# Kernel tuning notes

Measured on AMD Instinct MI355X. Metric: run time of the kernel, lower is better.

The kernel has to match this reference:

```python
import jax, jax.numpy as jnp
import numpy as np

HID = 768      # hidden_dim
HEADS = 12     # num_heads (each head projects HID -> HID, unsplit)
NP_ = 196      # num_patches = (224/16)^2
PATCH = 256    # 1*16*16
SEQ = NP_ + 1  # +CLS
OUT = 1000
BLOCKS = 6
EPS = 1e-5


def setup_inputs() -> dict:
    key = jax.random.key(0)
    ks = jax.random.split(key, 12)
    def w(k, shape, s=0.02):
        return jax.random.normal(k, shape, jnp.float32) * s
    return {
        "X": jax.random.normal(ks[0], (8, 1, 224, 224), jnp.float32),
        "W_patch": w(ks[1], (HID, PATCH)), "b_patch": jnp.zeros((HID,), jnp.float32),
        "cls_emb": jax.random.uniform(ks[2], (1, HID), jnp.float32),
        "pos_emb": jax.random.uniform(ks[3], (SEQ, HID), jnp.float32),
        "ln1_g": jnp.ones((SEQ, HID), jnp.float32), "ln1_b": jnp.zeros((SEQ, HID), jnp.float32),
        "Wq": w(ks[4], (HEADS, HID, HID)), "bq": jnp.zeros((HEADS, HID), jnp.float32),
        "Wk": w(ks[5], (HEADS, HID, HID)), "bk": jnp.zeros((HEADS, HID), jnp.float32),
        "Wv": w(ks[6], (HEADS, HID, HID)), "bv": jnp.zeros((HEADS, HID), jnp.float32),
        "Wo": w(ks[7], (HID, HEADS * HID)), "bo": jnp.zeros((HID,), jnp.float32),
        "ln2_g": jnp.ones((SEQ, HID), jnp.float32), "ln2_b": jnp.zeros((SEQ, HID), jnp.float32),
        "W2": w(ks[8], (HID, HID)), "b2": jnp.zeros((HID,), jnp.float32),
        "Wh": w(ks[9], (OUT, HID)), "bh": jnp.zeros((OUT,), jnp.float32),
    }


def _ln2d(x, g, b):
    # torch nn.LayerNorm((SEQ, HID)): normalize over the last TWO dims
    m = x.mean(axis=(-2, -1), keepdims=True)
    v = x.var(axis=(-2, -1), keepdims=True)
    return (x - m) / jnp.sqrt(v + EPS) * g + b


def reference(X, W_patch, b_patch, cls_emb, pos_emb, ln1_g, ln1_b,
              Wq, bq, Wk, bk, Wv, bv, Wo, bo, ln2_g, ln2_b, W2, b2, Wh, bh):
    N = X.shape[0]
    patches = X.reshape(N, NP_, PATCH)
    E = patches @ W_patch.T + b_patch                      # [N, 196, HID]
    cls = jnp.broadcast_to(cls_emb[None], (N, 1, HID))
    Z = jnp.concatenate([cls, E], axis=1) + pos_emb[None]  # [N, SEQ, HID]
    scale = 1.0 / (HID ** 2)                               # repo's unusual scaling
    for _ in range(BLOCKS):  # same weights reused each iteration (as in source)
        x = _ln2d(Z, ln1_g, ln1_b)
        # batched per-head full-width projections: Wq[h] is (out=e, in=d)
        q = jnp.einsum('nsd,hed->nhse', x, Wq) + bq[None, :, None, :]
        k = jnp.einsum('nsd,hed->nhse', x, Wk) + bk[None, :, None, :]
        v = jnp.einsum('nsd,hed->nhse', x, Wv) + bv[None, :, None, :]
        A = jax.nn.softmax(jnp.einsum('nhse,nhte->nhst', q, k) * scale, axis=-1)
        h = jnp.einsum('nhst,nhte->nhse', A, v)            # [N, HEADS, SEQ, HID]
        hcat = jnp.transpose(h, (0, 2, 1, 3)).reshape(N, SEQ, HEADS * HID)
        attn = hcat @ Wo.T + bo                            # [N, SEQ, HID]
        y = _ln2d(attn + Z, ln2_g, ln2_b)
        Z = y @ W2.T + b2                                  # note: no residual here (as in source)
    return jnp.tanh(Z[:, 0] @ Wh.T + bh)                   # [N, OUT]
```

## Files before the change

### kernel.cpp

```cpp
#include <hip/hip_runtime.h>
#include <hip/hip_bf16.h>
#include <math.h>

typedef __hip_bfloat16 bf16;
typedef __attribute__((ext_vector_type(8))) short short8;
typedef __attribute__((ext_vector_type(4))) float f32x4;

#define HIDD   768
#define SEQL   197
#define NPATCH 196
#define PATCHD 256
#define NHEADS 12
#define NBATCH 8
#define OUTDIM 1000
#define NBLOCKS 6
#define EPSV   1e-5f
#define HH     (NHEADS * HIDD)
#define M_ALL  (NBATCH * SEQL)
#define MPATCH (NBATCH * NPATCH)
#define PLD    256
#define KPV    224
#define KSPLIT 4

__device__ __forceinline__ unsigned short f2bf(float f) {
  union { bf16 h; unsigned short u; } cv; cv.h = __float2bfloat16(f); return cv.u;
}
__device__ __forceinline__ float bf2f(unsigned short u) {
  union { unsigned int i; float f; } w; w.i = ((unsigned int)u) << 16; return w.f;
}

typedef __attribute__((address_space(3))) unsigned int lds_uint;
typedef __attribute__((address_space(1))) const unsigned int g_uint;
__device__ __forceinline__ void gload16(const void* g, void* l) {
  __builtin_amdgcn_global_load_lds((g_uint*)g, (lds_uint*)l, 16, 0, 0);
}

__global__ __launch_bounds__(256) void cvt_bf(const float4* __restrict__ src,
                                              ushort4* __restrict__ dst, int n4) {
  for (int i = blockIdx.x * 256 + threadIdx.x; i < n4; i += gridDim.x * 256) {
    float4 v = src[i];
    ushort4 o;
    o.x = f2bf(v.x); o.y = f2bf(v.y); o.z = f2bf(v.z); o.w = f2bf(v.w);
    dst[i] = o;
  }
}

__global__ __launch_bounds__(256) void twk(const float* __restrict__ Wk,
                                           unsigned short* __restrict__ Wkt) {
  const long long idx = (long long)blockIdx.x * 256 + threadIdx.x;
  const int h = (int)(idx / (HIDD * HIDD));
  const int rem = (int)(idx - (long long)h * HIDD * HIDD);
  const int d = rem / HIDD, e = rem - d * HIDD;
  Wkt[idx] = f2bf(Wk[(long long)h * HIDD * HIDD + (long long)e * HIDD + d]);
}

__global__ __launch_bounds__(256) void cvec(const float* __restrict__ Wk,
    const float* __restrict__ bq, float* __restrict__ c) {
  const int h = blockIdx.z;
  const int dp = blockIdx.x * 256 + threadIdx.x;
  const float* W = Wk + (long long)h * HIDD * HIDD;
  const float* b = bq + h * HIDD;
  float s = 0.f;
  for (int e = 0; e < HIDD; ++e) s += W[(long long)e * HIDD + dp] * b[e];
  c[h * HIDD + dp] = s;
}

__global__ __launch_bounds__(256) void beff_k(const float* __restrict__ Wo,
    const float* __restrict__ bv, const float* __restrict__ bo,
    float* __restrict__ beff) {
  const int dout = blockIdx.x * 4 + (threadIdx.x >> 6);
  const int lane = threadIdx.x & 63;
  const float* row = Wo + (long long)dout * HH;
  float s = 0.f;
  for (int i = lane * 4; i < HH; i += 256) {
    float4 w = *(const float4*)(row + i);
    float4 b = *(const float4*)(bv + i);
    s += w.x * b.x + w.y * b.y + w.z * b.z + w.w * b.w;
  }
  for (int o = 32; o; o >>= 1) s += __shfl_xor(s, o, 64);
  if (lane == 0) beff[dout] = bo[dout] + s;
}

__global__ __launch_bounds__(256) void dcol(const unsigned short* __restrict__ Xn,
    const float* __restrict__ c, float* __restrict__ D) {
  const int z = blockIdx.x;
  const int n = z / NHEADS, h = z - n * NHEADS;
  const int wid = threadIdx.x >> 6, lane = threadIdx.x & 63;
  const float* ch = c + h * HIDD;
  float cc[3][4];
#pragma unroll
  for (int k = 0; k < 3; ++k)
    *(float4*)cc[k] = *(const float4*)(ch + k * 256 + lane * 4);
  const int t0 = blockIdx.y * 64 + wid * 16;
#pragma unroll
  for (int tt = 0; tt < 16; ++tt) {
    const int t = t0 + tt;
    float s = 0.f;
    if (t < SEQL) {
      const unsigned short* xr = Xn + (long long)(n * SEQL + t) * HIDD;
#pragma unroll
      for (int k = 0; k < 3; ++k) {
        ushort4 xv = *(const ushort4*)(xr + k * 256 + lane * 4);
        s += bf2f(xv.x) * cc[k][0] + bf2f(xv.y) * cc[k][1]
           + bf2f(xv.z) * cc[k][2] + bf2f(xv.w) * cc[k][3];
      }
    }
    for (int o = 32; o; o >>= 1) s += __shfl_xor(s, o, 64);
    if (lane == 0) D[z * 256 + t] = s;
  }
}

__global__ __launch_bounds__(256) void xpose(const unsigned short* __restrict__ Xn,
    unsigned short* __restrict__ Xt) {
  __shared__ unsigned short tile[64][72];
  const int n = blockIdx.z;
  const int e0 = blockIdx.x * 64, t0 = blockIdx.y * 64;
  const int tr = threadIdx.x >> 2;
  const int tc = (threadIdx.x & 3) * 16;
  const int t = t0 + tr;
#pragma unroll
  for (int j = 0; j < 2; ++j) {
    int4 v = {0, 0, 0, 0};
    if (t < SEQL)
      v = *(const int4*)(Xn + (long long)(n * SEQL + t) * HIDD + e0 + tc + j * 8);
    *(int4*)&tile[tr][tc + j * 8] = v;
  }
  __syncthreads();
  const int er = threadIdx.x >> 2;
  const int tcc = (threadIdx.x & 3) * 16;
  unsigned short tmp[16];
#pragma unroll
  for (int j = 0; j < 16; ++j) tmp[j] = tile[tcc + j][er];
  unsigned short* drow = Xt + ((long long)n * HIDD + e0 + er) * 256 + t0 + tcc;
  *(int4*)drow = *(int4*)&tmp[0];
  *(int4*)(drow + 8) = *(int4*)&tmp[8];
}

template<bool BF16C>
__global__ __launch_bounds__(512, 2) void gemm_8ph(
    const unsigned short* __restrict__ A, int lda,
    const unsigned short* __restrict__ B, int ldb,
    void* __restrict__ Cp, int ldc,
    const float* __restrict__ bias, float alpha,
    int M, int N, int K, int gy)
{
  __shared__ alignas(16) unsigned short Abuf[2 * 2 * 128 * 64];
  __shared__ alignas(16) unsigned short Bbuf[2 * 2 * 128 * 64];

  const int nwg = gridDim.x;
  const int qq = nwg >> 3, rr = nwg & 7;
  const int xcd = blockIdx.x & 7, wix = blockIdx.x >> 3;
  const int f = xcd * qq + (xcd < rr ? xcd : rr) + wix;
  const int m0 = (f % gy) * 256, n0 = (f / gy) * 256;

  const int tid = threadIdx.x;
  const int lane = tid & 63, wid = tid >> 6;
  const int wr = wid >> 2, wc = wid & 3;
  const int lr = lane & 15, g = lane >> 4;

  const int srow = tid >> 3;
  const int schunk = ((tid & 7) ^ ((tid >> 3) & 7)) * 8;
  const int wbyte = wid * 1024;
  const int axor = lr & 7;

  const int ktiles = K >> 6;

  f32x4 acc[8][4];
#pragma unroll
  for (int m = 0; m < 8; ++m)
#pragma unroll
    for (int n = 0; n < 4; ++n) acc[m][n] = (f32x4){0.f, 0.f, 0.f, 0.f};

  auto stA = [&](int kt, int h) {
    const unsigned short* src = A + (long long)(m0 + h * 128 + srow) * lda + kt * 64 + schunk;
    char* dst = (char*)Abuf + ((kt & 1) * 2 + h) * 16384 + wbyte;
    gload16(src, dst);
    gload16(src + 64ll * lda, dst + 8192);
  };
  auto stB = [&](int kt, int h) {
    const unsigned short* src = B + (long long)(n0 + h * 128 + srow) * ldb + kt * 64 + schunk;
    char* dst = (char*)Bbuf + ((kt & 1) * 2 + h) * 16384 + wbyte;
    gload16(src, dst);
    gload16(src + 64ll * ldb, dst + 8192);
  };

  stB(0, 0); stB(0, 1); stA(0, 0); stA(0, 1);
  __builtin_amdgcn_s_waitcnt(0x0F72);
  __builtin_amdgcn_sched_barrier(0);
  __builtin_amdgcn_s_barrier();
  __builtin_amdgcn_sched_barrier(0);

  for (int t = 0; t < ktiles; ++t) {
    const int d = t & 1;
    const char* Ab_ = (const char*)Abuf + (d * 2 + wr) * 16384;
    const char* Bb_ = (const char*)Bbuf + (d * 2 + (wc >> 1)) * 16384;
    const int brow = (wc & 1) * 64;
    const bool more = (t + 1 < ktiles);

    short8 a[4][2], bA[2][2], bB[2][2];

#pragma unroll
    for (int m = 0; m < 4; ++m)
#pragma unroll
      for (int ks = 0; ks < 2; ++ks)
        a[m][ks] = *(const short8*)(Ab_ + (m * 16 + lr) * 128 + ((((ks << 2) | g) ^ axor) << 4));
#pragma unroll
    for (int n = 0; n < 2; ++n)
#pragma unroll
      for (int ks = 0; ks < 2; ++ks)
        bA[n][ks] = *(const short8*)(Bb_ + (brow + n * 16 + lr) * 128 + ((((ks << 2) | g) ^ axor) << 4));
    if (more) stB(t + 1, 0);
    __builtin_amdgcn_sched_barrier(0);
    __builtin_amdgcn_s_barrier();
    __builtin_amdgcn_sched_barrier(0);
    __builtin_amdgcn_s_waitcnt(0xC07F);
    __builtin_amdgcn_sched_barrier(0);
    __builtin_amdgcn_s_setprio(1);
#pragma unroll
    for (int m = 0; m < 4; ++m)
#pragma unroll
      for (int n = 0; n < 2; ++n)
#pragma unroll
        for (int ks = 0; ks < 2; ++ks)
          acc[m][n] = __builtin_amdgcn_mfma_f32_16x16x32_bf16(a[m][ks], bA[n][ks], acc[m][n], 0, 0, 0);
    __builtin_amdgcn_s_setprio(0);
    __builtin_amdgcn_sched_barrier(0);
    __builtin_amdgcn_s_barrier();
    __builtin_amdgcn_sched_barrier(0);

#pragma unroll
    for (int n = 0; n < 2; ++n)
#pragma unroll
      for (int ks = 0; ks < 2; ++ks)
        bB[n][ks] = *(const short8*)(Bb_ + (brow + (n + 2) * 16 + lr) * 128 + ((((ks << 2) | g) ^ axor) << 4));
    if (more) stB(t + 1, 1);
    if (more) __builtin_amdgcn_s_waitcnt(0x0F74);
    else      __builtin_amdgcn_s_waitcnt(0x0F70);
    __builtin_amdgcn_sched_barrier(0);
    __builtin_amdgcn_s_barrier();
    __builtin_amdgcn_sched_barrier(0);
    __builtin_amdgcn_s_waitcnt(0xC07F);
    __builtin_amdgcn_sched_barrier(0);
    __builtin_amdgcn_s_setprio(1);
#pragma unroll
    for (int m = 0; m < 4; ++m)
#pragma unroll
      for (int n = 0; n < 2; ++n)
#pragma unroll
        for (int ks = 0; ks < 2; ++ks)
          acc[m][n + 2] = __builtin_amdgcn_mfma_f32_16x16x32_bf16(a[m][ks], bB[n][ks], acc[m][n + 2], 0, 0, 0);
    __builtin_amdgcn_s_setprio(0);
    __builtin_amdgcn_sched_barrier(0);
    __builtin_amdgcn_s_barrier();
    __builtin_amdgcn_sched_barrier(0);

#pragma unroll
    for (int m = 0; m < 4; ++m)
#pragma unroll
      for (int ks = 0; ks < 2; ++ks)
        a[m][ks] = *(const short8*)(Ab_ + (64 + m * 16 + lr) * 128 + ((((ks << 2) | g) ^ axor) << 4));
    if (more) stA(t + 1, 0);
    __builtin_amdgcn_sched_barrier(0);
    __builtin_amdgcn_s_barrier();
    __builtin_amdgcn_sched_barrier(0);
    __builtin_amdgcn_s_waitcnt(0xC07F);
    __builtin_amdgcn_sched_barrier(0);
    __builtin_amdgcn_s_setprio(1);
#pragma unroll
    for (int m = 0; m < 4; ++m)
#pragma unroll
      for (int n = 0; n < 2; ++n)
#pragma unroll
        for (int ks = 0; ks < 2; ++ks)
          acc[m + 4][n + 2] = __builtin_amdgcn_mfma_f32_16x16x32_bf16(a[m][ks], bB[n][ks], acc[m + 4][n + 2], 0, 0, 0);
    __builtin_amdgcn_s_setprio(0);
    __builtin_amdgcn_sched_barrier(0);
    __builtin_amdgcn_s_barrier();
    __builtin_amdgcn_sched_barrier(0);

    if (more) {
      stA(t + 1, 1);
      __builtin_amdgcn_s_waitcnt(0x0F72);
    }
    __builtin_amdgcn_sched_barrier(0);
    __builtin_amdgcn_s_barrier();
    __builtin_amdgcn_sched_barrier(0);
    __builtin_amdgcn_s_setprio(1);
#pragma unroll
    for (int m = 0; m < 4; ++m)
#pragma unroll
      for (int n = 0; n < 2; ++n)
#pragma unroll
        for (int ks = 0; ks < 2; ++ks)
          acc[m + 4][n] = __builtin_amdgcn_mfma_f32_16x16x32_bf16(a[m][ks], bA[n][ks], acc[m + 4][n], 0, 0, 0);
    __builtin_amdgcn_s_setprio(0);
    __builtin_amdgcn_sched_barrier(0);
    __builtin_amdgcn_s_barrier();
    __builtin_amdgcn_sched_barrier(0);
  }

#pragma unroll
  for (int m = 0; m < 8; ++m) {
#pragma unroll
    for (int n = 0; n < 4; ++n) {
      const int gn = n0 + wc * 64 + n * 16 + lr;
      const float bv = bias ? bias[gn] : 0.f;
#pragma unroll
      for (int r = 0; r < 4; ++r) {
        const int gm = m0 + wr * 128 + m * 16 + g * 4 + r;
        if (gm >= M) continue;
        const float v = acc[m][n][r] * alpha + bv;
        if constexpr (BF16C)
          ((unsigned short*)Cp)[(long long)gm * ldc + gn] = f2bf(v);
        else
          ((float*)Cp)[(long long)gm * ldc + gn] = v;
      }
    }
  }
}

template<int BM, int BN, int WGM, int WGN, bool BF16C>
__global__ __launch_bounds__(256, 2) void gemm_bt(
    const unsigned short* __restrict__ A, long long sAz1, long long sAz2, int lda,
    const unsigned short* __restrict__ B, long long sBz1, long long sBz2, int ldb,
    void* __restrict__ Cp, long long sCz1, long long sCz2, int ldc,
    const float* __restrict__ bias, int zdiv, float alpha,
    int M, int N, int K, int gy)
{
  constexpr int BK = 32;
  constexpr int VM = BM / 64 + BN / 64;
  static_assert(WGM * WGN == 4, "4 waves");
  __shared__ unsigned short As[3][BM * BK];
  __shared__ unsigned short Bs[3][BN * BK];

  const int z  = blockIdx.z;
  const int z1 = z / zdiv, z2 = z - z1 * zdiv;
  const unsigned short* Ab = A + z1 * sAz1 + z2 * sAz2;
  const unsigned short* Bb = B + z1 * sBz1 + z2 * sBz2;
  const long long coff = z1 * sCz1 + z2 * sCz2;

  const int nwg = gridDim.x;
  const int qq = nwg >> 3, rr = nwg & 7;
  const int xcd = blockIdx.x & 7, wix = blockIdx.x >> 3;
  const int f = xcd * qq + (xcd < rr ? xcd : rr) + wix;
  const int m0 = (f % gy) * BM, n0 = (f / gy) * BN;

  const int tid = threadIdx.x;
  const int lane = tid & 63, wid = tid >> 6;
  const int wr = wid / WGN, wc = wid % WGN;
  constexpr int WM = BM / WGM, WN = BN / WGN, TM = WM / 16, TN = WN / 16;
  const int lr = lane & 15, g = lane >> 4;

  const int sr = wid * 16 + (lane >> 2);
  const int sc = (((lane & 3) ^ ((lane >> 3) & 3)) * 8);
  const int wbyte = wid * 1024;

  f32x4 acc[TM][TN];
#pragma unroll
  for (int m = 0; m < TM; ++m)
#pragma unroll
    for (int n = 0; n < TN; ++n) acc[m][n] = (f32x4){0.f, 0.f, 0.f, 0.f};

  auto stage = [&](int bufi, int kt) {
    const int k0 = kt * BK;
#pragma unroll
    for (int u = 0; u < BM / 64; ++u)
      gload16(Ab + (long long)(m0 + u * 64 + sr) * lda + k0 + sc,
              (char*)&As[bufi][0] + u * 4096 + wbyte);
#pragma unroll
    for (int u = 0; u < BN / 64; ++u)
      gload16(Bb + (long long)(n0 + u * 64 + sr) * ldb + k0 + sc,
              (char*)&Bs[bufi][0] + u * 4096 + wbyte);
  };

  const int rchunk = (g ^ ((lr >> 1) & 3)) * 8;

  const int ktiles = K / BK;
  stage(0, 0);
  if (ktiles > 1) stage(1, 1);
  int cur = 0;
  for (int t = 0; t < ktiles; ++t) {
    if (t + 1 < ktiles) __builtin_amdgcn_s_waitcnt(0x0F70 | VM);
    else                __builtin_amdgcn_s_waitcnt(0x0F70);
    __builtin_amdgcn_s_barrier();
    if (t + 2 < ktiles) {
      int nb = cur + 2; if (nb >= 3) nb -= 3;
      stage(nb, t + 2);
    }
    __builtin_amdgcn_sched_barrier(0);

    short8 a[TM], b[TN];
#pragma unroll
    for (int m = 0; m < TM; ++m)
      a[m] = *(const short8*)&As[cur][(wr * WM + m * 16 + lr) * BK + rchunk];
#pragma unroll
    for (int n = 0; n < TN; ++n)
      b[n] = *(const short8*)&Bs[cur][(wc * WN + n * 16 + lr) * BK + rchunk];
#pragma unroll
    for (int m = 0; m < TM; ++m)
#pragma unroll
      for (int n = 0; n < TN; ++n)
        acc[m][n] = __builtin_amdgcn_mfma_f32_16x16x32_bf16(a[m], b[n], acc[m][n], 0, 0, 0);
    cur = (cur == 2) ? 0 : cur + 1;
  }

#pragma unroll
  for (int m = 0; m < TM; ++m) {
#pragma unroll
    for (int n = 0; n < TN; ++n) {
      const int gn = n0 + wc * WN + n * 16 + lr;
      if (gn >= N) continue;
      const float bv = bias ? bias[gn] : 0.f;
#pragma unroll
      for (int r = 0; r < 4; ++r) {
        const int gm = m0 + wr * WM + m * 16 + g * 4 + r;
        if (gm >= M) continue;
        const float v = acc[m][n][r] * alpha + bv;
        if constexpr (BF16C)
          ((unsigned short*)Cp)[coff + (long long)gm * ldc + gn] = f2bf(v);
        else
          ((float*)Cp)[coff + (long long)gm * ldc + gn] = v;
      }
    }
  }
}

__global__ __launch_bounds__(256, 2) void scores_sm(
    const unsigned short* __restrict__ U, const unsigned short* __restrict__ Xn,
    const float* __restrict__ Dv, unsigned short* __restrict__ P, float scale)
{
  constexpr int BK = 32;
  __shared__ unsigned short As[3][64 * BK];
  __shared__ unsigned short Bs[3][256 * BK];

  const int z  = blockIdx.z;
  const int z1 = z / NHEADS, z2 = z - z1 * NHEADS;
  const unsigned short* Ab = U + (long long)z1 * SEQL * HH + (long long)z2 * HIDD;
  const unsigned short* Bb = Xn + (long long)z1 * SEQL * HIDD;
  unsigned short* Pz = P + (long long)z * SEQL * PLD;

  const int m0 = blockIdx.x * 64;
  const int tid = threadIdx.x;
  const int lane = tid & 63, wid = tid >> 6;
  const int lr = lane & 15, g = lane >> 4;

  const int sr = wid * 16 + (lane >> 2);
  const int sc = (((lane & 3) ^ ((lane >> 3) & 3)) * 8);
  const int wbyte = wid * 1024;
  const int rchunk = (g ^ ((lr >> 1) & 3)) * 8;

  f32x4 acc[16];
#pragma unroll
  for (int n = 0; n < 16; ++n) acc[n] = (f32x4){0.f, 0.f, 0.f, 0.f};

  auto stage = [&](int bufi, int kt) {
    const int k0 = kt * BK;
    gload16(Ab + (long long)(m0 + sr) * HH + k0 + sc, (char*)&As[bufi][0] + wbyte);
#pragma unroll
    for (int u = 0; u < 4; ++u)
      gload16(Bb + (long long)(u * 64 + sr) * HIDD + k0 + sc,
              (char*)&Bs[bufi][0] + u * 4096 + wbyte);
  };

  const int ktiles = HIDD / BK;
  stage(0, 0);
  stage(1, 1);
  int cur = 0;
  for (int t = 0; t < ktiles; ++t) {
    if (t + 1 < ktiles) __builtin_amdgcn_s_waitcnt(0x0F75);
    else                __builtin_amdgcn_s_waitcnt(0x0F70);
    __builtin_amdgcn_s_barrier();
    if (t + 2 < ktiles) {
      int nb = cur + 2; if (nb >= 3) nb -= 3;
      stage(nb, t + 2);
    }
    __builtin_amdgcn_sched_barrier(0);

    short8 a = *(const short8*)&As[cur][(wid * 16 + lr) * BK + rchunk];
#pragma unroll
    for (int n = 0; n < 16; ++n) {
      short8 b = *(const short8*)&Bs[cur][(n * 16 + lr) * BK + rchunk];
      acc[n] = __builtin_amdgcn_mfma_f32_16x16x32_bf16(a, b, acc[n], 0, 0, 0);
    }
    cur = (cur == 2) ? 0 : cur + 1;
  }

  const float* Dz = Dv + z * 256;
  float dv[16];
#pragma unroll
  for (int n = 0; n < 16; ++n) dv[n] = Dz[n * 16 + lr];

  const int growb = m0 + wid * 16 + g * 4;
#pragma unroll
  for (int r = 0; r < 4; ++r) {
    float mx = -1e30f;
#pragma unroll
    for (int n = 0; n < 16; ++n)
      if (n * 16 + lr < SEQL) mx = fmaxf(mx, (acc[n][r] + dv[n]) * scale);
    for (int o = 1; o < 16; o <<= 1) mx = fmaxf(mx, __shfl_xor(mx, o, 64));
    float sum = 0.f;
#pragma unroll
    for (int n = 0; n < 16; ++n) {
      const float e = (n * 16 + lr < SEQL) ? __expf((acc[n][r] + dv[n]) * scale - mx) : 0.f;
      acc[n][r] = e;
      sum += e;
    }
    for (int o = 1; o < 16; o <<= 1) sum += __shfl_xor(sum, o, 64);
    const float inv = 1.f / sum;
    const int grow = growb + r;
    if (grow < SEQL) {
#pragma unroll
      for (int n = 0; n < 16; ++n)
        Pz[(long long)grow * PLD + n * 16 + lr] = f2bf(acc[n][r] * inv);
    }
  }
}

template<int BM, int BN, bool BF16C>
__global__ __launch_bounds__(256) void gemm_nn(
    const unsigned short* __restrict__ A, long long sAz1, long long sAz2, int lda,
    const unsigned short* __restrict__ Bb, long long sBz1, long long sBz2, int ldb,
    void* __restrict__ Cp, long long sCz1, long long sCz2, int ldc,
    const float* __restrict__ bias, int zdiv, float alpha,
    int M, int N, int K, int Kvalid)
{
  constexpr int BK = 32;
  constexpr int LP = 40;
  __shared__ unsigned short As[BM * LP];
  __shared__ unsigned short Bs[BN * LP];

  const int z  = blockIdx.z;
  const int z1 = z / zdiv, z2 = z - z1 * zdiv;
  const unsigned short* Ab = A + z1 * sAz1 + z2 * sAz2;
  const unsigned short* Bp = Bb + z1 * sBz1 + z2 * sBz2;
  const long long coff = z1 * sCz1 + z2 * sCz2;

  const int tid = threadIdx.x;
  const int m0 = blockIdx.y * BM, n0 = blockIdx.x * BN;
  const int lane = tid & 63, wid = tid >> 6;
  const int wr = wid >> 1, wc = wid & 1;
  constexpr int WM = BM / 2, WN = BN / 2, TM = WM / 16, TN = WN / 16;
  const int lr = lane & 15, g = lane >> 4;
  const int srow = tid >> 2, scg = tid & 3;

  f32x4 acc[TM][TN];
#pragma unroll
  for (int m = 0; m < TM; ++m)
#pragma unroll
    for (int n = 0; n < TN; ++n) acc[m][n] = (f32x4){0.f, 0.f, 0.f, 0.f};

  for (int k0 = 0; k0 < K; k0 += BK) {
#pragma unroll
    for (int u = 0; u < BM / 64; ++u) {
      const int row = u * 64 + srow;
      const int gm = m0 + row;
      int4 val = {0, 0, 0, 0};
      if (gm < M)
        val = *(const int4*)(Ab + (long long)gm * lda + k0 + scg * 8);
      *(int4*)&As[row * LP + scg * 8] = val;
    }
    {
      constexpr int CH = BN / 8;
      constexpr int KP = BK / 2;
      static_assert(KP * CH <= 256, "staging exceeds block");
      if (tid < KP * CH) {
        const int kp = tid / CH;
        const int c8 = (tid - kp * CH) * 8;
        const int gn = n0 + c8;
        const int gk0 = k0 + 2 * kp;
        unsigned short r0[8] = {0,0,0,0,0,0,0,0};
        unsigned short r1[8] = {0,0,0,0,0,0,0,0};
        if (gk0 < Kvalid) {
          if (gn + 7 < N) *(int4*)r0 = *(const int4*)(Bp + (long long)gk0 * ldb + gn);
          else { for (int j = 0; j < 8; ++j) if (gn + j < N) r0[j] = Bp[(long long)gk0 * ldb + gn + j]; }
        }
        if (gk0 + 1 < Kvalid) {
          if (gn + 7 < N) *(int4*)r1 = *(const int4*)(Bp + (long long)(gk0 + 1) * ldb + gn);
          else { for (int j = 0; j < 8; ++j) if (gn + j < N) r1[j] = Bp[(long long)(gk0 + 1) * ldb + gn + j]; }
        }
#pragma unroll
        for (int j = 0; j < 8; ++j)
          *(unsigned int*)&Bs[(c8 + j) * LP + 2 * kp] =
              (unsigned int)r0[j] | ((unsigned int)r1[j] << 16);
      }
    }
    __syncthreads();

    short8 a[TM], b[TN];
#pragma unroll
    for (int m = 0; m < TM; ++m)
      a[m] = *(const short8*)&As[(wr * WM + m * 16 + lr) * LP + g * 8];
#pragma unroll
    for (int n = 0; n < TN; ++n)
      b[n] = *(const short8*)&Bs[(wc * WN + n * 16 + lr) * LP + g * 8];
#pragma unroll
    for (int m = 0; m < TM; ++m)
#pragma unroll
      for (int n = 0; n < TN; ++n)
        acc[m][n] = __builtin_amdgcn_mfma_f32_16x16x32_bf16(a[m], b[n], acc[m][n], 0, 0, 0);
    __syncthreads();
  }

#pragma unroll
  for (int m = 0; m < TM; ++m) {
#pragma unroll
    for (int n = 0; n < TN; ++n) {
      const int gn = n0 + wc * WN + n * 16 + lr;
      if (gn >= N) continue;
      const float bv = bias ? bias[gn] : 0.f;
#pragma unroll
      for (int r = 0; r < 4; ++r) {
        const int gm = m0 + wr * WM + m * 16 + g * 4 + r;
        if (gm >= M) continue;
        const float v = acc[m][n][r] * alpha + bv;
        if constexpr (BF16C)
          ((unsigned short*)Cp)[coff + (long long)gm * ldc + gn] = f2bf(v);
        else
          ((float*)Cp)[coff + (long long)gm * ldc + gn] = v;
      }
    }
  }
}

template<int BM, int BN>
__global__ __launch_bounds__(256) void gemm_k(
    const float* __restrict__ A, long long sAz1, int lda,
    const float* __restrict__ B, int ldb,
    float* __restrict__ C, long long sCz1, int ldc,
    const float* __restrict__ bias,
    const float* __restrict__ resid, int ldr,
    float alpha, int M, int N, int K, int act)
{
  constexpr int BK = 16;
  constexpr int TM = BM / 16;
  constexpr int TN = BN / 16;
  __shared__ float As[BK][BM];
  __shared__ float Bs[BK][BN];

  const int z = blockIdx.z;
  A += z * sAz1;
  C += z * sCz1;
  const float* R = resid;

  const int tid = threadIdx.x;
  const int tx = tid & 15, ty = tid >> 4;
  const int m0 = blockIdx.y * BM, n0 = blockIdx.x * BN;

  float acc[TM][TN];
#pragma unroll
  for (int i = 0; i < TM; ++i)
#pragma unroll
    for (int j = 0; j < TN; ++j) acc[i][j] = 0.f;

  for (int k0 = 0; k0 < K; k0 += BK) {
    {
      constexpr int AV = (BM * BK / 4) / 256;
#pragma unroll
      for (int u = 0; u < AV; ++u) {
        const int vi = tid + u * 256;
        const int r  = vi / (BK / 4);
        const int c4 = (vi % (BK / 4)) * 4;
        const int gm = m0 + r, gk = k0 + c4;
        float4 v = {0.f, 0.f, 0.f, 0.f};
        if (gm < M) v = *(const float4*)(A + (long long)gm * lda + gk);
        As[c4 + 0][r] = v.x; As[c4 + 1][r] = v.y;
        As[c4 + 2][r] = v.z; As[c4 + 3][r] = v.w;
      }
    }
    {
      constexpr int BV = (BN * BK / 4) / 256;
#pragma unroll
      for (int u = 0; u < BV; ++u) {
        const int vi = tid + u * 256;
        const int r  = vi / (BK / 4);
        const int c4 = (vi % (BK / 4)) * 4;
        const int gn = n0 + r, gk = k0 + c4;
        float4 v = {0.f, 0.f, 0.f, 0.f};
        if (gn < N) v = *(const float4*)(B + (long long)gn * ldb + gk);
        Bs[c4 + 0][r] = v.x; Bs[c4 + 1][r] = v.y;
        Bs[c4 + 2][r] = v.z; Bs[c4 + 3][r] = v.w;
      }
    }
    __syncthreads();
#pragma unroll
    for (int kk = 0; kk < BK; ++kk) {
      float a[TM], bb[TN];
#pragma unroll
      for (int i = 0; i < TM; i += 4)
        *reinterpret_cast<float4*>(&a[i]) = *reinterpret_cast<const float4*>(&As[kk][ty * TM + i]);
#pragma unroll
      for (int j = 0; j < TN; j += 4)
        *reinterpret_cast<float4*>(&bb[j]) = *reinterpret_cast<const float4*>(&Bs[kk][tx * TN + j]);
#pragma unroll
      for (int i = 0; i < TM; ++i)
#pragma unroll
        for (int j = 0; j < TN; ++j) acc[i][j] = fmaf(a[i], bb[j], acc[i][j]);
    }
    __syncthreads();
  }

#pragma unroll
  for (int i = 0; i < TM; ++i) {
    const int gm = m0 + ty * TM + i;
    if (gm >= M) continue;
#pragma unroll
    for (int j = 0; j < TN; ++j) {
      const int gn = n0 + tx * TN + j;
      if (gn >= N) continue;
      float v = acc[i][j] * alpha;
      if (bias) v += bias[gn];
      if (R)    v += R[(long long)gm * ldr + gn];
      if (act)  v = tanhf(v);
      C[(long long)gm * ldc + gn] = v;
    }
  }
}

__global__ __launch_bounds__(256) void embed_merge(
    const float* __restrict__ Etmp, const float* __restrict__ cls,
    const float* __restrict__ pos, float* __restrict__ Z)
{
  const int tot = NBATCH * SEQL * HIDD / 4;
  for (int i = blockIdx.x * 256 + threadIdx.x; i < tot; i += gridDim.x * 256) {
    const int n  = i / (SEQL * HIDD / 4);
    const int se = i - n * (SEQL * HIDD / 4);
    const int s  = se / (HIDD / 4);
    const int e4 = se - s * (HIDD / 4);
    float4 pv = ((const float4*)pos)[se];
    float4 src;
    if (s == 0) src = ((const float4*)cls)[e4];
    else        src = ((const float4*)Etmp)[(long long)(n * NPATCH + s - 1) * (HIDD / 4) + e4];
    float4 o;
    o.x = src.x + pv.x; o.y = src.y + pv.y;
    o.z = src.z + pv.z; o.w = src.w + pv.w;
    ((float4*)Z)[i] = o;
  }
}

__global__ __launch_bounds__(256) void ln_part(const float* __restrict__ x, float* __restrict__ part) {
  const int b = blockIdx.x;
  const int n = b >> 4, seg = b & 15;
  const int per = (SEQL * HIDD / 4) / 16;
  const float4* px = (const float4*)(x + (size_t)n * SEQL * HIDD);
  float s = 0.f, q = 0.f;
  for (int i = seg * per + threadIdx.x; i < (seg + 1) * per; i += 256) {
    float4 v = px[i];
    s += v.x + v.y + v.z + v.w;
    q += v.x * v.x + v.y * v.y + v.z * v.z + v.w * v.w;
  }
  for (int o = 32; o; o >>= 1) { s += __shfl_xor(s, o, 64); q += __shfl_xor(q, o, 64); }
  __shared__ float ls[8];
  const int wid = threadIdx.x >> 6, lane = threadIdx.x & 63;
  if (lane == 0) { ls[wid] = s; ls[4 + wid] = q; }
  __syncthreads();
  if (threadIdx.x == 0) {
    part[b] = ls[0] + ls[1] + ls[2] + ls[3];
    part[128 + b] = ls[4] + ls[5] + ls[6] + ls[7];
  }
}

__global__ __launch_bounds__(256) void wo_ln_part(
    const float4* __restrict__ Cp, const float4* __restrict__ Z4,
    const float4* __restrict__ bo4, float4* __restrict__ out4,
    float* __restrict__ part)
{
  const int b = blockIdx.x;
  const int n = b >> 4, seg = b & 15;
  const int per = (SEQL * HIDD / 4) / 16;
  const int tot = M_ALL * HIDD / 4;
  const long long base = (long long)n * (SEQL * HIDD / 4);
  float s = 0.f, q = 0.f;
  for (int i = seg * per + threadIdx.x; i < (seg + 1) * per; i += 256) {
    const long long gi = base + i;
    float4 a = Cp[gi], b2 = Cp[tot + gi], c = Cp[2 * tot + gi], d = Cp[3 * tot + gi];
    float4 zv = Z4[gi];
    float4 bb = bo4[i % (HIDD / 4)];
    float4 o;
    o.x = a.x + b2.x + c.x + d.x + zv.x + bb.x;
    o.y = a.y + b2.y + c.y + d.y + zv.y + bb.y;
    o.z = a.z + b2.z + c.z + d.z + zv.z + bb.z;
    o.w = a.w + b2.w + c.w + d.w + zv.w + bb.w;
    out4[gi] = o;
    s += o.x + o.y + o.z + o.w;
    q += o.x * o.x + o.y * o.y + o.z * o.z + o.w * o.w;
  }
  for (int o = 32; o; o >>= 1) { s += __shfl_xor(s, o, 64); q += __shfl_xor(q, o, 64); }
  __shared__ float ls[8];
  const int wid = threadIdx.x >> 6, lane = threadIdx.x & 63;
  if (lane == 0) { ls[wid] = s; ls[4 + wid] = q; }
  __syncthreads();
  if (threadIdx.x == 0) {
    part[b] = ls[0] + ls[1] + ls[2] + ls[3];
    part[128 + b] = ls[4] + ls[5] + ls[6] + ls[7];
  }
}

__global__ __launch_bounds__(256) void ln_apply_bf(const float* __restrict__ x,
    const float* __restrict__ g, const float* __restrict__ b,
    const float* __restrict__ part, unsigned short* __restrict__ y)
{
  __shared__ float ms[8], rs[8];
  if (threadIdx.x < 8) {
    const int n = threadIdx.x;
    float s = 0.f, qv = 0.f;
    for (int j = 0; j < 16; ++j) { s += part[n * 16 + j]; qv += part[128 + n * 16 + j]; }
    const float inv = 1.f / (float)(SEQL * HIDD);
    const float m = s * inv;
    ms[n] = m;
    rs[n] = rsqrtf(qv * inv - m * m + EPSV);
  }
  __syncthreads();
  const int tot = NBATCH * SEQL * HIDD / 4;
  for (int i = blockIdx.x * 256 + threadIdx.x; i < tot; i += gridDim.x * 256) {
    const int n  = i / (SEQL * HIDD / 4);
    const int se = i - n * (SEQL * HIDD / 4);
    const float m = ms[n], r = rs[n];
    float4 xv = ((const float4*)x)[i];
    float4 gv = ((const float4*)g)[se];
    float4 bv = ((const float4*)b)[se];
    ushort4 o;
    o.x = f2bf((xv.x - m) * r * gv.x + bv.x);
    o.y = f2bf((xv.y - m) * r * gv.y + bv.y);
    o.z = f2bf((xv.z - m) * r * gv.z + bv.z);
    o.w = f2bf((xv.w - m) * r * gv.w + bv.w);
    ((ushort4*)y)[i] = o;
  }
}

extern "C" void kernel_launch(void* const* d_in, const int* in_sizes, int n_in,
                              void* d_out, int out_size, void* d_ws, size_t ws_size,
                              hipStream_t stream)
{
  const float* X    = (const float*)d_in[0];
  const float* Wp   = (const float*)d_in[1];
  const float* bp   = (const float*)d_in[2];
  const float* cls  = (const float*)d_in[3];
  const float* pos  = (const float*)d_in[4];
  const float* ln1g = (const float*)d_in[5];
  const float* ln1b = (const float*)d_in[6];
  const float* Wq   = (const float*)d_in[7];
  const float* bq   = (const float*)d_in[8];
  const float* Wk   = (const float*)d_in[9];
  const float* bk   = (const float*)d_in[10];
  const float* Wv   = (const float*)d_in[11];
  const float* bv   = (const float*)d_in[12];
  const float* Wo   = (const float*)d_in[13];
  const float* bo   = (const float*)d_in[14];
  const float* ln2g = (const float*)d_in[15];
  const float* ln2b = (const float*)d_in[16];
  const float* W2   = (const float*)d_in[17];
  const float* b2   = (const float*)d_in[18];
  const float* Wh   = (const float*)d_in[19];
  const float* bh   = (const float*)d_in[20];
  float* out = (float*)d_out;
  (void)in_sizes; (void)n_in; (void)out_size; (void)ws_size;

  char* base = (char*)d_ws;
  size_t off = 0;
  auto alloc = [&](size_t bytes) -> char* {
    char* r = base + off;
    off += (bytes + 255) & ~(size_t)255;
    return r;
  };
  const size_t ZB  = (size_t)M_ALL * HIDD * 4;
  const size_t XB  = (size_t)M_ALL * HIDD * 2;
  const size_t DB  = (size_t)NBATCH * NHEADS * 256 * 4;
  const size_t PB  = (size_t)NBATCH * NHEADS * SEQL * PLD * 2;
  const size_t XTB = (size_t)NBATCH * HIDD * 256 * 2;
  const size_t UB  = (size_t)M_ALL * HH * 2;
  const size_t MTB = (size_t)HH * HIDD * 2;
  const size_t CPB = (size_t)KSPLIT * M_ALL * HIDD * 4;
  const size_t FTB = (size_t)HIDD * HH * 4;

  float*          Z     = (float*)alloc(ZB);
  float*          Ares  = (float*)alloc(ZB);
  unsigned short* Xnb   = (unsigned short*)alloc(XB);
  float*          stats = (float*)alloc(4096);
  float*          Dbuf  = (float*)alloc(DB);
  unsigned short* Pb    = (unsigned short*)alloc(PB);
  unsigned short* Xt    = (unsigned short*)alloc(XTB);
  unsigned short* U     = (unsigned short*)alloc(UB);
  unsigned short* Mt_bf = (unsigned short*)alloc(MTB);
  unsigned short* Gcat  = (unsigned short*)alloc(MTB);
  unsigned short* W2_bf = (unsigned short*)alloc((size_t)HIDD * HIDD * 2);
  float*          cvecb = (float*)alloc((size_t)NHEADS * HIDD * 4);
  float*          beff  = (float*)alloc((size_t)HIDD * 4);
  float*          Cpart = (float*)alloc(CPB);
  float*          Ftmp  = (float*)alloc(FTB);

  unsigned short* Wq_bf = U;
  unsigned short* Wkt   = U + (size_t)HH * HIDD;
  unsigned short* Wv_bf = (unsigned short*)Cpart;
  unsigned short* Wo_bf = (unsigned short*)base;
  unsigned short* Xbf   = Pb;
  unsigned short* Wp_bf = Pb + 425984;
  float*          Etmp  = Cpart;

  const float scale = 1.0f / ((float)HIDD * (float)HIDD);
  const long long sUn = (long long)SEQL * HH;
  const long long sPn = (long long)NHEADS * SEQL * PLD;
  const long long sPh = (long long)SEQL * PLD;
  const int WO4 = HH * HIDD / 4, W24 = HIDD * HIDD / 4;

  cvt_bf<<<dim3(4096), 256, 0, stream>>>((const float4*)Wq, (ushort4*)Wq_bf, WO4);
  twk<<<dim3(NHEADS * HIDD * HIDD / 256), 256, 0, stream>>>(Wk, Wkt);
  gemm_nn<64, 128, false><<<dim3(HIDD / 128, HIDD / 64, NHEADS), 256, 0, stream>>>(
      Wkt, 0, (long long)HIDD * HIDD, HIDD,
      Wq_bf, 0, (long long)HIDD * HIDD, HIDD,
      Ftmp, 0, (long long)HIDD * HIDD, HIDD,
      nullptr, NHEADS, 1.0f, HIDD, HIDD, HIDD, HIDD);
  cvt_bf<<<dim3(4096), 256, 0, stream>>>((const float4*)Ftmp, (ushort4*)Mt_bf, WO4);
  cvec<<<dim3(3, 1, NHEADS), 256, 0, stream>>>(Wk, bq, cvecb);
  cvt_bf<<<dim3(4096), 256, 0, stream>>>((const float4*)Wv, (ushort4*)Wv_bf, WO4);
  cvt_bf<<<dim3(4096), 256, 0, stream>>>((const float4*)Wo, (ushort4*)Wo_bf, WO4);
  gemm_nn<64, 128, false><<<dim3(HIDD / 128, HIDD / 64, NHEADS), 256, 0, stream>>>(
      Wo_bf, 0, (long long)HIDD, HH,
      Wv_bf, 0, (long long)HIDD * HIDD, HIDD,
      Ftmp, 0, (long long)HIDD, HH,
      nullptr, NHEADS, 1.0f, HIDD, HIDD, HIDD, HIDD);
  cvt_bf<<<dim3(4096), 256, 0, stream>>>((const float4*)Ftmp, (ushort4*)Gcat, WO4);
  beff_k<<<dim3(HIDD / 4), 256, 0, stream>>>(Wo, bv, bo, beff);
  cvt_bf<<<dim3(512), 256, 0, stream>>>((const float4*)W2, (ushort4*)W2_bf, W24);
  cvt_bf<<<dim3(392), 256, 0, stream>>>((const float4*)X,  (ushort4*)Xbf,  MPATCH * PATCHD / 4);
  cvt_bf<<<dim3(192), 256, 0, stream>>>((const float4*)Wp, (ushort4*)Wp_bf, HIDD * PATCHD / 4);
  gemm_bt<64, 64, 2, 2, false><<<dim3(25 * (HIDD / 64), 1, 1), 256, 0, stream>>>(
      Xbf, 0, 0, PATCHD, Wp_bf, 0, 0, PATCHD, Etmp, 0, 0, HIDD,
      bp, 1, 1.0f, MPATCH, HIDD, PATCHD, 25);
  embed_merge<<<dim3(1182), 256, 0, stream>>>(Etmp, cls, pos, Z);

  for (int blk = 0; blk < NBLOCKS; ++blk) {
    ln_part<<<dim3(128), 256, 0, stream>>>(Z, stats);
    ln_apply_bf<<<dim3(1182), 256, 0, stream>>>(Z, ln1g, ln1b, stats, Xnb);

    dcol<<<dim3(NBATCH * NHEADS, 4), 256, 0, stream>>>(Xnb, cvecb, Dbuf);
    xpose<<<dim3(HIDD / 64, 4, NBATCH), 256, 0, stream>>>(Xnb, Xt);

    gemm_8ph<true><<<dim3((HH / 256) * 7, 1, 1), 512, 0, stream>>>(
        Xnb, HIDD, Mt_bf, HIDD, U, HH,
        nullptr, 1.0f, M_ALL, HH, HIDD, 7);

    scores_sm<<<dim3(4, 1, NBATCH * NHEADS), 256, 0, stream>>>(
        U, Xnb, Dbuf, Pb, scale);

    gemm_bt<64, 64, 2, 2, true><<<dim3(4 * (HIDD / 64), 1, NBATCH * NHEADS), 256, 0, stream>>>(
        Pb, sPn, sPh, PLD,
        Xt, (long long)HIDD * 256, 0, 256,
        U, sUn, HIDD, HH,
        nullptr, NHEADS, 1.0f, SEQL, HIDD, KPV, 4);

    gemm_bt<64, 64, 2, 2, false><<<dim3(25 * (HIDD / 64), 1, KSPLIT), 256, 0, stream>>>(
        U, 0, HH / KSPLIT, HH,
        Gcat, 0, HH / KSPLIT, HH,
        Cpart, 0, (long long)M_ALL * HIDD, HIDD,
        nullptr, KSPLIT, 1.0f, M_ALL, HIDD, HH / KSPLIT, 25);

    wo_ln_part<<<dim3(128), 256, 0, stream>>>(
        (const float4*)Cpart, (const float4*)Z, (const float4*)beff, (float4*)Ares, stats);
    ln_apply_bf<<<dim3(1182), 256, 0, stream>>>(Ares, ln2g, ln2b, stats, Xnb);

    gemm_bt<64, 64, 2, 2, false><<<dim3(25 * (HIDD / 64), 1, 1), 256, 0, stream>>>(
        Xnb, 0, 0, HIDD, W2_bf, 0, 0, HIDD, Z, 0, 0, HIDD,
        b2, 1, 1.0f, M_ALL, HIDD, HIDD, 25);
  }

  gemm_k<64, 64><<<dim3((OUTDIM + 63) / 64, 1, 1), 256, 0, stream>>>(
      Z, 0, SEQL * HIDD,
      Wh, HIDD,
      out, 0, OUTDIM,
      bh, nullptr, 0,
      1.0f, NBATCH, OUTDIM, HIDD, 1);
}
```

Baseline: 1.556 ms.

## Precompute fused weight products via tiled transposes and bf16-output gemm_bt

The weight preprocessing (Wk^T·Wq and Wo·Wv products) now builds transposed bf16 weights with an LDS-tiled transpose kernel, then uses the existing gemm_bt kernel with direct bf16 output. This drops the gemm_nn kernel, the fp32 Ftmp intermediate, and its extra conversion passes. The bias-vector kernel now reads the transposed bf16 Wk with coalesced warp reductions instead of strided fp32 columns. The cost is a small precision change, since cvec is now computed from bf16 weights, and an extra transpose launch for Wq and Wv.

```diff
diff --git a/kernel.cpp b/kernel.cpp
--- a/kernel.cpp
+++ b/kernel.cpp
@@ -45,24 +45,48 @@
   }
 }
 
-__global__ __launch_bounds__(256) void twk(const float* __restrict__ Wk,
-                                           unsigned short* __restrict__ Wkt) {
-  const long long idx = (long long)blockIdx.x * 256 + threadIdx.x;
-  const int h = (int)(idx / (HIDD * HIDD));
-  const int rem = (int)(idx - (long long)h * HIDD * HIDD);
-  const int d = rem / HIDD, e = rem - d * HIDD;
-  Wkt[idx] = f2bf(Wk[(long long)h * HIDD * HIDD + (long long)e * HIDD + d]);
-}
-
-__global__ __launch_bounds__(256) void cvec(const float* __restrict__ Wk,
+__global__ __launch_bounds__(256) void wtrans(const float* __restrict__ S,
+    unsigned short* __restrict__ Dst) {
+  __shared__ unsigned short tile[64][72];
+  const int h = blockIdx.z;
+  const int c0 = blockIdx.x * 64, r0 = blockIdx.y * 64;
+  const long long base = (long long)h * HIDD * HIDD;
+  const int tr = threadIdx.x >> 2;
+  const int tc = (threadIdx.x & 3) * 16;
+#pragma unroll
+  for (int j = 0; j < 4; ++j) {
+    float4 v = *(const float4*)(S + base + (long long)(r0 + tr) * HIDD + c0 + tc + j * 4);
+    tile[tr][tc + j * 4 + 0] = f2bf(v.x);
+    tile[tr][tc + j * 4 + 1] = f2bf(v.y);
+    tile[tr][tc + j * 4 + 2] = f2bf(v.z);
+    tile[tr][tc + j * 4 + 3] = f2bf(v.w);
+  }
+  __syncthreads();
+  const int er = threadIdx.x >> 2;
+  const int ec = (threadIdx.x & 3) * 16;
+  unsigned short tmp[16];
+#pragma unroll
+  for (int j = 0; j < 16; ++j) tmp[j] = tile[ec + j][er];
+  unsigned short* drow = Dst + ((long long)h * HIDD + c0 + er) * HIDD + r0 + ec;
+  *(int4*)drow = *(int4*)&tmp[0];
+  *(int4*)(drow + 8) = *(int4*)&tmp[8];
+}
+
+__global__ __launch_bounds__(256) void cvec2(const unsigned short* __restrict__ Wkt,
     const float* __restrict__ bq, float* __restrict__ c) {
-  const int h = blockIdx.z;
-  const int dp = blockIdx.x * 256 + threadIdx.x;
-  const float* W = Wk + (long long)h * HIDD * HIDD;
+  const int h = blockIdx.y;
+  const int dp = blockIdx.x * 4 + (threadIdx.x >> 6);
+  const int lane = threadIdx.x & 63;
+  const unsigned short* row = Wkt + ((long long)h * HIDD + dp) * HIDD;
   const float* b = bq + h * HIDD;
   float s = 0.f;
-  for (int e = 0; e < HIDD; ++e) s += W[(long long)e * HIDD + dp] * b[e];
-  c[h * HIDD + dp] = s;
+  for (int e = lane * 4; e < HIDD; e += 256) {
+    ushort4 w = *(const ushort4*)(row + e);
+    s += bf2f(w.x) * b[e] + bf2f(w.y) * b[e + 1]
+       + bf2f(w.z) * b[e + 2] + bf2f(w.w) * b[e + 3];
+  }
+  for (int o = 32; o; o >>= 1) s += __shfl_xor(s, o, 64);
+  if (lane == 0) c[h * HIDD + dp] = s;
 }
 
 __global__ __launch_bounds__(256) void beff_k(const float* __restrict__ Wo,
@@ -512,112 +536,6 @@
 #pragma unroll
       for (int n = 0; n < 16; ++n)
         Pz[(long long)grow * PLD + n * 16 + lr] = f2bf(acc[n][r] * inv);
-    }
-  }
-}
-
-template<int BM, int BN, bool BF16C>
-__global__ __launch_bounds__(256) void gemm_nn(
-    const unsigned short* __restrict__ A, long long sAz1, long long sAz2, int lda,
-    const unsigned short* __restrict__ Bb, long long sBz1, long long sBz2, int ldb,
-    void* __restrict__ Cp, long long sCz1, long long sCz2, int ldc,
-    const float* __restrict__ bias, int zdiv, float alpha,
-    int M, int N, int K, int Kvalid)
-{
-  constexpr int BK = 32;
-  constexpr int LP = 40;
-  __shared__ unsigned short As[BM * LP];
-  __shared__ unsigned short Bs[BN * LP];
-
-  const int z  = blockIdx.z;
-  const int z1 = z / zdiv, z2 = z - z1 * zdiv;
-  const unsigned short* Ab = A + z1 * sAz1 + z2 * sAz2;
-  const unsigned short* Bp = Bb + z1 * sBz1 + z2 * sBz2;
-  const long long coff = z1 * sCz1 + z2 * sCz2;
-
-  const int tid = threadIdx.x;
-  const int m0 = blockIdx.y * BM, n0 = blockIdx.x * BN;
-  const int lane = tid & 63, wid = tid >> 6;
-  const int wr = wid >> 1, wc = wid & 1;
-  constexpr int WM = BM / 2, WN = BN / 2, TM = WM / 16, TN = WN / 16;
-  const int lr = lane & 15, g = lane >> 4;
-  const int srow = tid >> 2, scg = tid & 3;
-
-  f32x4 acc[TM][TN];
-#pragma unroll
-  for (int m = 0; m < TM; ++m)
-#pragma unroll
-    for (int n = 0; n < TN; ++n) acc[m][n] = (f32x4){0.f, 0.f, 0.f, 0.f};
-
-  for (int k0 = 0; k0 < K; k0 += BK) {
-#pragma unroll
-    for (int u = 0; u < BM / 64; ++u) {
-      const int row = u * 64 + srow;
-      const int gm = m0 + row;
-      int4 val = {0, 0, 0, 0};
-      if (gm < M)
-        val = *(const int4*)(Ab + (long long)gm * lda + k0 + scg * 8);
-      *(int4*)&As[row * LP + scg * 8] = val;
-    }
-    {
-      constexpr int CH = BN / 8;
-      constexpr int KP = BK / 2;
-      static_assert(KP * CH <= 256, "staging exceeds block");
-      if (tid < KP * CH) {
-        const int kp = tid / CH;
-        const int c8 = (tid - kp * CH) * 8;
-        const int gn = n0 + c8;
-        const int gk0 = k0 + 2 * kp;
-        unsigned short r0[8] = {0,0,0,0,0,0,0,0};
-        unsigned short r1[8] = {0,0,0,0,0,0,0,0};
-        if (gk0 < Kvalid) {
-          if (gn + 7 < N) *(int4*)r0 = *(const int4*)(Bp + (long long)gk0 * ldb + gn);
-          else { for (int j = 0; j < 8; ++j) if (gn + j < N) r0[j] = Bp[(long long)gk0 * ldb + gn + j]; }
-        }
-        if (gk0 + 1 < Kvalid) {
-          if (gn + 7 < N) *(int4*)r1 = *(const int4*)(Bp + (long long)(gk0 + 1) * ldb + gn);
-          else { for (int j = 0; j < 8; ++j) if (gn + j < N) r1[j] = Bp[(long long)(gk0 + 1) * ldb + gn + j]; }
-        }
-#pragma unroll
-        for (int j = 0; j < 8; ++j)
-          *(unsigned int*)&Bs[(c8 + j) * LP + 2 * kp] =
-              (unsigned int)r0[j] | ((unsigned int)r1[j] << 16);
-      }
-    }
-    __syncthreads();
-
-    short8 a[TM], b[TN];
-#pragma unroll
-    for (int m = 0; m < TM; ++m)
-      a[m] = *(const short8*)&As[(wr * WM + m * 16 + lr) * LP + g * 8];
-#pragma unroll
-    for (int n = 0; n < TN; ++n)
-      b[n] = *(const short8*)&Bs[(wc * WN + n * 16 + lr) * LP + g * 8];
-#pragma unroll
-    for (int m = 0; m < TM; ++m)
-#pragma unroll
-      for (int n = 0; n < TN; ++n)
-        acc[m][n] = __builtin_amdgcn_mfma_f32_16x16x32_bf16(a[m], b[n], acc[m][n], 0, 0, 0);
-    __syncthreads();
-  }
-
-#pragma unroll
-  for (int m = 0; m < TM; ++m) {
-#pragma unroll
-    for (int n = 0; n < TN; ++n) {
-      const int gn = n0 + wc * WN + n * 16 + lr;
-      if (gn >= N) continue;
-      const float bv = bias ? bias[gn] : 0.f;
-#pragma unroll
-      for (int r = 0; r < 4; ++r) {
-        const int gm = m0 + wr * WM + m * 16 + g * 4 + r;
-        if (gm >= M) continue;
-        const float v = acc[m][n][r] * alpha + bv;
-        if constexpr (BF16C)
-          ((unsigned short*)Cp)[coff + (long long)gm * ldc + gn] = f2bf(v);
-        else
-          ((float*)Cp)[coff + (long long)gm * ldc + gn] = v;
-      }
     }
   }
 }
@@ -870,7 +788,6 @@
   const size_t UB  = (size_t)M_ALL * HH * 2;
   const size_t MTB = (size_t)HH * HIDD * 2;
   const size_t CPB = (size_t)KSPLIT * M_ALL * HIDD * 4;
-  const size_t FTB = (size_t)HIDD * HH * 4;
 
   float*          Z     = (float*)alloc(ZB);
   float*          Ares  = (float*)alloc(ZB);
@@ -886,11 +803,10 @@
   float*          cvecb = (float*)alloc((size_t)NHEADS * HIDD * 4);
   float*          beff  = (float*)alloc((size_t)HIDD * 4);
   float*          Cpart = (float*)alloc(CPB);
-  float*          Ftmp  = (float*)alloc(FTB);
-
-  unsigned short* Wq_bf = U;
-  unsigned short* Wkt   = U + (size_t)HH * HIDD;
-  unsigned short* Wv_bf = (unsigned short*)Cpart;
+
+  unsigned short* Wkt   = U;
+  unsigned short* Wqt   = U + (size_t)NHEADS * HIDD * HIDD;
+  unsigned short* Wvt   = (unsigned short*)Cpart;
   unsigned short* Wo_bf = (unsigned short*)base;
   unsigned short* Xbf   = Pb;
   unsigned short* Wp_bf = Pb + 425984;
@@ -900,25 +816,24 @@
   const long long sUn = (long long)SEQL * HH;
   const long long sPn = (long long)NHEADS * SEQL * PLD;
   const long long sPh = (long long)SEQL * PLD;
-  const int WO4 = HH * HIDD / 4, W24 = HIDD * HIDD / 4;
-
-  cvt_bf<<<dim3(4096), 256, 0, stream>>>((const float4*)Wq, (ushort4*)Wq_bf, WO4);
-  twk<<<dim3(NHEADS * HIDD * HIDD / 256), 256, 0, stream>>>(Wk, Wkt);
-  gemm_nn<64, 128, false><<<dim3(HIDD / 128, HIDD / 64, NHEADS), 256, 0, stream>>>(
-      Wkt, 0, (long long)HIDD * HIDD, HIDD,
-      Wq_bf, 0, (long long)HIDD * HIDD, HIDD,
-      Ftmp, 0, (long long)HIDD * HIDD, HIDD,
-      nullptr, NHEADS, 1.0f, HIDD, HIDD, HIDD, HIDD);
-  cvt_bf<<<dim3(4096), 256, 0, stream>>>((const float4*)Ftmp, (ushort4*)Mt_bf, WO4);
-  cvec<<<dim3(3, 1, NHEADS), 256, 0, stream>>>(Wk, bq, cvecb);
-  cvt_bf<<<dim3(4096), 256, 0, stream>>>((const float4*)Wv, (ushort4*)Wv_bf, WO4);
-  cvt_bf<<<dim3(4096), 256, 0, stream>>>((const float4*)Wo, (ushort4*)Wo_bf, WO4);
-  gemm_nn<64, 128, false><<<dim3(HIDD / 128, HIDD / 64, NHEADS), 256, 0, stream>>>(
-      Wo_bf, 0, (long long)HIDD, HH,
-      Wv_bf, 0, (long long)HIDD * HIDD, HIDD,
-      Ftmp, 0, (long long)HIDD, HH,
-      nullptr, NHEADS, 1.0f, HIDD, HIDD, HIDD, HIDD);
-  cvt_bf<<<dim3(4096), 256, 0, stream>>>((const float4*)Ftmp, (ushort4*)Gcat, WO4);
+  const long long HH2 = (long long)HIDD * HIDD;
+  const int W24 = HIDD * HIDD / 4;
+
+  wtrans<<<dim3(12, 12, NHEADS), 256, 0, stream>>>(Wk, Wkt);
+  wtrans<<<dim3(12, 12, NHEADS), 256, 0, stream>>>(Wq, Wqt);
+  wtrans<<<dim3(12, 12, NHEADS), 256, 0, stream>>>(Wv, Wvt);
+  gemm_bt<64, 64, 2, 2, true><<<dim3(144, 1, NHEADS), 256, 0, stream>>>(
+      Wkt, 0, HH2, HIDD,
+      Wqt, 0, HH2, HIDD,
+      Mt_bf, 0, HH2, HIDD,
+      nullptr, NHEADS, 1.0f, HIDD, HIDD, HIDD, 12);
+  cvec2<<<dim3(HIDD / 4, NHEADS), 256, 0, stream>>>(Wkt, bq, cvecb);
+  cvt_bf<<<dim3(4096), 256, 0, stream>>>((const float4*)Wo, (ushort4*)Wo_bf, HH * HIDD / 4);
+  gemm_bt<64, 64, 2, 2, true><<<dim3(144, 1, NHEADS), 256, 0, stream>>>(
+      Wo_bf, 0, HIDD, HH,
+      Wvt, 0, HH2, HIDD,
+      Gcat, 0, HIDD, HH,
+      nullptr, NHEADS, 1.0f, HIDD, HIDD, HIDD, 12);
   beff_k<<<dim3(HIDD / 4), 256, 0, stream>>>(Wo, bv, bo, beff);
   cvt_bf<<<dim3(512), 256, 0, stream>>>((const float4*)W2, (ushort4*)W2_bf, W24);
   cvt_bf<<<dim3(392), 256, 0, stream>>>((const float4*)X,  (ushort4*)Xbf,  MPATCH * PATCHD / 4);
```

After: 1.396 ms. 10.2% less time.
